# Kernel optimization log

Hardware: AMD Instinct MI355X
Metric: run time of the kernel (lower is better)

## Reference

```python
import jax, jax.numpy as jnp
import numpy as np

NUM_GROUPS = 32
EPS = 1e-6
NUM_HEADS = 8
HEAD_DIM = 64


def group_norm(x, gamma, beta):
    # x: [B, C, H, W]
    B, C, H, W = x.shape
    xg = x.reshape(B, NUM_GROUPS, C // NUM_GROUPS, H, W)
    mean = xg.mean(axis=(2, 3, 4), keepdims=True)
    var = xg.var(axis=(2, 3, 4), keepdims=True)
    xn = ((xg - mean) * jax.lax.rsqrt(var + EPS)).reshape(B, C, H, W)
    return xn * gamma[None, :, None, None] + beta[None, :, None, None]


def setup_inputs() -> dict:
    key = jax.random.key(0)
    ks = jax.random.split(key, 4)
    B, C, H, W = 8, 512, 32, 32
    hid = NUM_HEADS * HEAD_DIM  # 512
    x = jax.random.normal(ks[0], (B, C, H, W), dtype=jnp.float32)
    gamma = jnp.ones((C,), dtype=jnp.float32)
    beta = jnp.zeros((C,), dtype=jnp.float32)
    w_in = jax.random.normal(ks[1], (3 * hid, C), dtype=jnp.float32) * (1.0 / np.sqrt(C))
    b_in = jnp.zeros((3 * hid,), dtype=jnp.float32)
    w_out = jax.random.normal(ks[2], (C, hid), dtype=jnp.float32) * (1.0 / np.sqrt(hid))
    b_out = jnp.zeros((C,), dtype=jnp.float32)
    return {"x": x, "gamma": gamma, "beta": beta, "w_in": w_in, "b_in": b_in,
            "w_out": w_out, "b_out": b_out}


def reference(x, gamma, beta, w_in, b_in, w_out, b_out):
    B, C, H, W = x.shape
    n, c = NUM_HEADS, HEAD_DIM
    skip = x
    h = group_norm(x, gamma, beta)
    # 1x1 conv proj_in: [B, 3*n*c, H, W]
    qkv = jnp.einsum('oc,bchw->bohw', w_in, h) + b_in[None, :, None, None]
    qkv = qkv.reshape(B, 3, n, c, H * W)
    q, k, v = qkv[:, 0], qkv[:, 1], qkv[:, 2]  # each [B, n, c, HW]
    scale = 1.0 / np.sqrt(c)
    logits = jnp.einsum('bncq,bnck->bnqk', q, k) * scale  # [B, n, HW, HW]
    w = jax.nn.softmax(logits, axis=-1)
    out = jnp.einsum('bnqk,bnck->bncq', w, v)  # [B, n, c, HW]
    out = out.reshape(B, n * c, H, W)
    out = jnp.einsum('oc,bchw->bohw', w_out, out) + b_out[None, :, None, None]
    return out + skip
```

## Files before the change

kernel.cpp:

```cpp
#include <hip/hip_runtime.h>
#include <hip/hip_bf16.h>

#define B_    8
#define C_    512
#define HW_   1024
#define NG    32
#define GCH   16
#define EPSV  1e-6f

typedef __attribute__((ext_vector_type(8))) short short8;
typedef __attribute__((ext_vector_type(4))) short short4v;
typedef __attribute__((ext_vector_type(4))) float floatx4;

static __device__ __forceinline__ short f2bs(float f) {
  return __builtin_bit_cast(short, __float2bfloat16(f));
}
static __device__ __forceinline__ short4v pack4(float a, float b, float c, float d) {
  return (short4v){f2bs(a), f2bs(b), f2bs(c), f2bs(d)};
}
static __device__ __forceinline__ unsigned pk2(float a, float b) {
  return (unsigned)(unsigned short)f2bs(a) |
         ((unsigned)(unsigned short)f2bs(b) << 16);
}
#define MFMA(a, b, c) __builtin_amdgcn_mfma_f32_16x16x32_bf16((a), (b), (c), 0, 0, 0)

static __device__ __forceinline__ void glds16(const short* g, short* l) {
  __builtin_amdgcn_global_load_lds(
      (const __attribute__((address_space(1))) void*)g,
      (__attribute__((address_space(3))) void*)l, 16, 0, 0);
}

__global__ __launch_bounds__(256) void gn_cast_fused(
    const float* __restrict__ x, const float* __restrict__ gamma,
    const float* __restrict__ beta, short* __restrict__ ht,
    const float* __restrict__ w_in, short* __restrict__ wbf1,
    const float* __restrict__ w_out, short* __restrict__ wbf2) {
  int blk = blockIdx.x;
  int t = threadIdx.x;

  if (blk >= 256) {
    int i = (blk - 256) * 256 + t;
    const float* s; short* d; int j;
    if (i < 196608) { s = w_in; d = wbf1; j = i; }
    else            { s = w_out; d = wbf2; j = i - 196608; }
    float4 v = reinterpret_cast<const float4*>(s)[j];
    reinterpret_cast<short4v*>(d)[j] = pack4(v.x, v.y, v.z, v.w);
    return;
  }

  int b = blk >> 5, g = blk & 31;
  const float* xp = x + ((size_t)(b * C_) + g * GCH) * HW_;

  __shared__ float Ls[4 * 1040];
  __shared__ float rs_[4], rss_[4], st_[2];

  float s = 0.f, ss = 0.f;
  for (int i = 0; i < 16; i++) {
    float4 v = *reinterpret_cast<const float4*>(xp + (t + i * 256) * 4);
    s  += (v.x + v.y) + (v.z + v.w);
    ss += (v.x * v.x + v.y * v.y) + (v.z * v.z + v.w * v.w);
  }
  for (int o = 32; o > 0; o >>= 1) {
    s  += __shfl_down(s, o);
    ss += __shfl_down(ss, o);
  }
  int wid = t >> 6, lane = t & 63;
  if (lane == 0) { rs_[wid] = s; rss_[wid] = ss; }
  __syncthreads();
  if (t == 0) {
    float stot  = rs_[0] + rs_[1] + rs_[2] + rs_[3];
    float sstot = rss_[0] + rss_[1] + rss_[2] + rss_[3];
    float mean = stot / 16384.f;
    float var  = sstot / 16384.f - mean * mean;
    st_[0] = mean;
    st_[1] = rsqrtf(var + EPSV);
  }
  __syncthreads();

  int r = t >> 4, c4 = t & 15;
  int ch = g * GCH + r;
  float ga = gamma[ch] * st_[1];
  float be = beta[ch] - st_[0] * ga;
  int sq = t >> 2, cq = t & 3;

  for (int it = 0; it < 4; it++) {
    for (int sub = 0; sub < 4; sub++) {
      int s0 = (it * 4 + sub) * 64;
      float4 v = *reinterpret_cast<const float4*>(xp + r * HW_ + s0 + c4 * 4);
      float* L = Ls + sub * 1040;
      L[r * 65 + c4 * 4 + 0] = v.x * ga + be;
      L[r * 65 + c4 * 4 + 1] = v.y * ga + be;
      L[r * 65 + c4 * 4 + 2] = v.z * ga + be;
      L[r * 65 + c4 * 4 + 3] = v.w * ga + be;
    }
    __syncthreads();
    for (int sub = 0; sub < 4; sub++) {
      int s0 = (it * 4 + sub) * 64;
      const float* L = Ls + sub * 1040;
      float a0 = L[(cq * 4 + 0) * 65 + sq];
      float a1 = L[(cq * 4 + 1) * 65 + sq];
      float a2 = L[(cq * 4 + 2) * 65 + sq];
      float a3 = L[(cq * 4 + 3) * 65 + sq];
      *reinterpret_cast<short4v*>(
          ht + ((size_t)b * 1024 + s0 + sq) * 512 + g * GCH + cq * 4) =
          pack4(a0, a1, a2, a3);
    }
    __syncthreads();
  }
}

__global__ __launch_bounds__(256) void gemm_qkv(
    const short* __restrict__ Wb, const short* __restrict__ ht,
    const float* __restrict__ bias,
    short* __restrict__ Qt, short* __restrict__ Kt, short* __restrict__ Vn) {
  __shared__ short As[2][4096];
  __shared__ short Bs[2][4096];
  int bx = blockIdx.x, by = blockIdx.y, bb = blockIdx.z;
  int m0 = by * 128, n0 = bx * 128;
  int t = threadIdx.x;
  int w = t >> 6, lane = t & 63, n16 = lane & 15, quad = lane >> 4;
  int wm = (w >> 1) * 64, wn = (w & 1) * 64;

  const short* Wa = Wb + (size_t)(m0 + (t >> 2)) * 512 + (t & 3) * 8;
  const short* Xa = ht + (size_t)bb * 1024 * 512 +
                    (size_t)(n0 + (t >> 2)) * 512 + (t & 3) * 8;

#define STAGE(buf, kk)                                                \
  do {                                                                \
    glds16(Wa + (kk), &As[buf][t * 8]);                               \
    glds16(Wa + 64 * 512 + (kk), &As[buf][2048 + t * 8]);             \
    glds16(Xa + (kk), &Bs[buf][t * 8]);                               \
    glds16(Xa + 64 * 512 + (kk), &Bs[buf][2048 + t * 8]);             \
  } while (0)

  floatx4 acc[4][4];
  for (int i = 0; i < 4; i++)
    for (int j = 0; j < 4; j++) acc[i][j] = (floatx4){0.f, 0.f, 0.f, 0.f};

  STAGE(0, 0);
#pragma unroll 1
  for (int ks = 0; ks < 16; ks++) {
    int cur = ks & 1;
    __syncthreads();
    if (ks < 15) STAGE(cur ^ 1, (ks + 1) * 32);
    short8 a[4], b[4];
    for (int im = 0; im < 4; im++)
      a[im] = *reinterpret_cast<const short8*>(
          &As[cur][(wm + im * 16 + n16) * 32 + quad * 8]);
    for (int in = 0; in < 4; in++)
      b[in] = *reinterpret_cast<const short8*>(
          &Bs[cur][(wn + in * 16 + n16) * 32 + quad * 8]);
    for (int im = 0; im < 4; im++)
      for (int in = 0; in < 4; in++)
        acc[im][in] = MFMA(a[im], b[in], acc[im][in]);
  }
#undef STAGE

  if (m0 < 1024) {
    const bool isQ = (m0 < 512);
    short* base = isQ ? Qt : Kt;
    const float sc = isQ ? 0.125f : 1.0f;
    for (int im = 0; im < 4; im++) {
      int m = m0 + wm + im * 16 + quad * 4;
      int hh = (m >> 6) & 7, d0 = m & 63;
      float4 bi = *reinterpret_cast<const float4*>(&bias[m]);
      short* hb = base + (size_t)(bb * 8 + hh) * 1024 * 64 + d0;
      for (int in = 0; in < 4; in++) {
        int nn = n0 + wn + in * 16 + n16;
        *reinterpret_cast<short4v*>(hb + (size_t)nn * 64) =
            pack4((acc[im][in][0] + bi.x) * sc, (acc[im][in][1] + bi.y) * sc,
                  (acc[im][in][2] + bi.z) * sc, (acc[im][in][3] + bi.w) * sc);
      }
    }
  } else {
    for (int im = 0; im < 4; im++) {
      int m = m0 + wm + im * 16 + quad * 4;
      float4 bi = *reinterpret_cast<const float4*>(&bias[m]);
      int ch = m - 1024;
      for (int in = 0; in < 4; in++) {
        int nn = n0 + wn + in * 16 + n16;
        short* vp = Vn + (size_t)(bb * 512 + ch) * 1024 + nn;
        vp[0]    = f2bs(acc[im][in][0] + bi.x);
        vp[1024] = f2bs(acc[im][in][1] + bi.y);
        vp[2048] = f2bs(acc[im][in][2] + bi.z);
        vp[3072] = f2bs(acc[im][in][3] + bi.w);
      }
    }
  }
}

__global__ __launch_bounds__(256)
__attribute__((amdgpu_waves_per_eu(2))) void attn_mfma(
    const short* __restrict__ Qt, const short* __restrict__ Kt,
    const short* __restrict__ Vn, short* __restrict__ attnT) {
  int blk0 = blockIdx.x;
  int blk = (blk0 & 7) * 64 + (blk0 >> 3);
  int qb = blk & 7, h = (blk >> 3) & 7, b = blk >> 6;
  int t = threadIdx.x;
  int w = t >> 6, lane = t & 63, n16 = lane & 15, quad = lane >> 4;
  int q0 = qb * 128 + w * 32;
  int qhi = quad >> 1;
  int srcA = ((quad & 1) << 5) + n16;
  int srcB = srcA + 16;

  const short* Qp = Qt + (size_t)(b * 8 + h) * 1024 * 64;
  const short* Kp = Kt + (size_t)(b * 8 + h) * 1024 * 64;
  const short* Vp = Vn + (size_t)(b * 512 + h * 64) * 1024;

  short8 qa[2][2];
  for (int qt = 0; qt < 2; qt++)
    for (int f = 0; f < 2; f++)
      qa[qt][f] = *reinterpret_cast<const short8*>(
          Qp + (size_t)(q0 + qt * 16 + n16) * 64 + f * 32 + quad * 8);

  floatx4 O[2][4];
  float l[2] = {0.f, 0.f};
  for (int qt = 0; qt < 2; qt++)
    for (int i = 0; i < 4; i++) O[qt][i] = (floatx4){0.f, 0.f, 0.f, 0.f};

  short8 kf[8][2];
  short8 vv[4][2];

#pragma unroll 1
  for (int kt = 0; kt < 8; kt++) {
    int k0 = kt * 128;
#pragma unroll
    for (int nt = 0; nt < 8; nt++)
#pragma unroll
      for (int f = 0; f < 2; f++)
        kf[nt][f] = *reinterpret_cast<const short8*>(
            Kp + (size_t)(k0 + nt * 16 + n16) * 64 + f * 32 + quad * 8);

    short8 pa[2][4];
#pragma unroll
    for (int qt = 0; qt < 2; qt++) {
      floatx4 T[8];
#pragma unroll
      for (int nt = 0; nt < 8; nt++) {
        floatx4 s_ = (floatx4){0.f, 0.f, 0.f, 0.f};
        s_ = MFMA(kf[nt][0], qa[qt][0], s_);
        T[nt] = MFMA(kf[nt][1], qa[qt][1], s_);
      }
      unsigned u[8][2];
#pragma unroll
      for (int nt = 0; nt < 8; nt++) {
        float p0 = __expf(T[nt][0]);
        float p1 = __expf(T[nt][1]);
        float p2 = __expf(T[nt][2]);
        float p3 = __expf(T[nt][3]);
        l[qt] += (p0 + p1) + (p2 + p3);
        u[nt][0] = pk2(p0, p1);
        u[nt][1] = pk2(p2, p3);
      }
#pragma unroll
      for (int fr = 0; fr < 4; fr++) {
        unsigned a0 = (unsigned)__shfl((int)u[2 * fr + 0][0], srcA);
        unsigned a1 = (unsigned)__shfl((int)u[2 * fr + 1][0], srcA);
        unsigned b0 = (unsigned)__shfl((int)u[2 * fr + 0][1], srcA);
        unsigned b1 = (unsigned)__shfl((int)u[2 * fr + 1][1], srcA);
        unsigned c0 = (unsigned)__shfl((int)u[2 * fr + 0][0], srcB);
        unsigned c1 = (unsigned)__shfl((int)u[2 * fr + 1][0], srcB);
        unsigned d0 = (unsigned)__shfl((int)u[2 * fr + 0][1], srcB);
        unsigned d1 = (unsigned)__shfl((int)u[2 * fr + 1][1], srcB);
        uint4 wv;
        wv.x = qhi ? a1 : a0;
        wv.y = qhi ? b1 : b0;
        wv.z = qhi ? c1 : c0;
        wv.w = qhi ? d1 : d0;
        pa[qt][fr] = __builtin_bit_cast(short8, wv);
      }
    }

#pragma unroll
    for (int half = 0; half < 2; half++) {
#pragma unroll
      for (int nd = 0; nd < 4; nd++) {
        const short* vs = Vp + (size_t)(nd * 16 + n16) * 1024 + k0 +
                          half * 64 + quad * 8;
        vv[nd][0] = *reinterpret_cast<const short8*>(vs);
        vv[nd][1] = *reinterpret_cast<const short8*>(vs + 32);
      }
      __builtin_amdgcn_s_setprio(1);
#pragma unroll
      for (int qt = 0; qt < 2; qt++)
#pragma unroll
        for (int nd = 0; nd < 4; nd++) {
          O[qt][nd] = MFMA(pa[qt][2 * half + 0], vv[nd][0], O[qt][nd]);
          O[qt][nd] = MFMA(pa[qt][2 * half + 1], vv[nd][1], O[qt][nd]);
        }
      __builtin_amdgcn_s_setprio(0);
    }
  }

  for (int qt = 0; qt < 2; qt++) {
    float s = l[qt];
    s += __shfl_xor(s, 16);
    s += __shfl_xor(s, 32);
    for (int nd = 0; nd < 4; nd++)
      for (int r = 0; r < 4; r++) {
        float linv = 1.0f / __shfl(s, quad * 4 + r);
        int q = q0 + qt * 16 + quad * 4 + r;
        int ch = h * 64 + nd * 16 + n16;
        attnT[((size_t)b * 1024 + q) * 512 + ch] = f2bs(O[qt][nd][r] * linv);
      }
  }
}

__global__ __launch_bounds__(256) void gemm_out(
    const short* __restrict__ Wb, const short* __restrict__ Xt,
    const float* __restrict__ bias, const float* __restrict__ resid,
    float* __restrict__ out) {
  __shared__ short As[2][2048];
  __shared__ short Bs[2][2048];
  int bx = blockIdx.x, by = blockIdx.y, bb = blockIdx.z;
  int m0 = by * 64, n0 = bx * 64;
  int t = threadIdx.x;
  int w = t >> 6, lane = t & 63, n16 = lane & 15, quad = lane >> 4;
  int wm = (w >> 1) * 32, wn = (w & 1) * 32;

  const short* Wa = Wb + (size_t)(m0 + (t >> 2)) * 512 + (t & 3) * 8;
  const short* Xa = Xt + (size_t)bb * 1024 * 512 +
                    (size_t)(n0 + (t >> 2)) * 512 + (t & 3) * 8;

#define STAGE(buf, kk)                                                \
  do {                                                                \
    glds16(Wa + (kk), &As[buf][t * 8]);                               \
    glds16(Xa + (kk), &Bs[buf][t * 8]);                               \
  } while (0)

  floatx4 acc[2][2];
  for (int i = 0; i < 2; i++)
    for (int j = 0; j < 2; j++) acc[i][j] = (floatx4){0.f, 0.f, 0.f, 0.f};

  STAGE(0, 0);
#pragma unroll 1
  for (int ks = 0; ks < 16; ks++) {
    int cur = ks & 1;
    __syncthreads();
    if (ks < 15) STAGE(cur ^ 1, (ks + 1) * 32);
    short8 a[2], b[2];
    for (int im = 0; im < 2; im++)
      a[im] = *reinterpret_cast<const short8*>(
          &As[cur][(wm + im * 16 + n16) * 32 + quad * 8]);
    for (int in = 0; in < 2; in++)
      b[in] = *reinterpret_cast<const short8*>(
          &Bs[cur][(wn + in * 16 + n16) * 32 + quad * 8]);
    for (int im = 0; im < 2; im++)
      for (int in = 0; in < 2; in++)
        acc[im][in] = MFMA(a[im], b[in], acc[im][in]);
  }
#undef STAGE

  for (int im = 0; im < 2; im++) {
    int m = m0 + wm + im * 16 + quad * 4;
    float4 bi = *reinterpret_cast<const float4*>(&bias[m]);
    for (int in = 0; in < 2; in++) {
      int nn = n0 + wn + in * 16 + n16;
      size_t idx = ((size_t)bb * 512 + m) * 1024 + nn;
      out[idx]        = acc[im][in][0] + bi.x + resid[idx];
      out[idx + 1024] = acc[im][in][1] + bi.y + resid[idx + 1024];
      out[idx + 2048] = acc[im][in][2] + bi.z + resid[idx + 2048];
      out[idx + 3072] = acc[im][in][3] + bi.w + resid[idx + 3072];
    }
  }
}

extern "C" void kernel_launch(void* const* d_in, const int* in_sizes, int n_in,
                              void* d_out, int out_size, void* d_ws, size_t ws_size,
                              hipStream_t stream) {
  const float* x     = (const float*)d_in[0];
  const float* gamma = (const float*)d_in[1];
  const float* beta  = (const float*)d_in[2];
  const float* w_in  = (const float*)d_in[3];
  const float* b_in  = (const float*)d_in[4];
  const float* w_out = (const float*)d_in[5];
  const float* b_out = (const float*)d_in[6];
  float* out = (float*)d_out;

  char* ws = (char*)d_ws;
  short* ht    = (short*)ws;
  short* Qt    = (short*)(ws + (8u  << 20));
  short* Kt    = (short*)(ws + (16u << 20));
  short* Vn    = (short*)(ws + (24u << 20));
  short* attnT = (short*)(ws + (32u << 20));
  short* wbf1  = (short*)(ws + (40u << 20));
  short* wbf2  = (short*)(ws + (42u << 20));

  gn_cast_fused<<<1280, 256, 0, stream>>>(x, gamma, beta, ht,
                                          w_in, wbf1, w_out, wbf2);
  gemm_qkv<<<dim3(8, 12, B_), 256, 0, stream>>>(wbf1, ht, b_in, Qt, Kt, Vn);
  attn_mfma<<<512, 256, 0, stream>>>(Qt, Kt, Vn, attnT);
  gemm_out<<<dim3(16, 8, B_), 256, 0, stream>>>(wbf2, attnT, b_out, x, out);
}
```

Before: 184.6 us.

## Stage K/V tiles in swizzled LDS with double buffering in attention

```diff
diff --git a/kernel.cpp b/kernel.cpp
--- a/kernel.cpp
+++ b/kernel.cpp
@@ -189,16 +189,17 @@
   }
 }
 
-__global__ __launch_bounds__(256)
-__attribute__((amdgpu_waves_per_eu(2))) void attn_mfma(
+__global__ __launch_bounds__(256) void attn_mfma(
     const short* __restrict__ Qt, const short* __restrict__ Kt,
     const short* __restrict__ Vn, short* __restrict__ attnT) {
+  __shared__ short KT[2][4096];
+  __shared__ short VT[2][4096];
   int blk0 = blockIdx.x;
-  int blk = (blk0 & 7) * 64 + (blk0 >> 3);
-  int qb = blk & 7, h = (blk >> 3) & 7, b = blk >> 6;
+  int blk = (blk0 & 7) * 128 + (blk0 >> 3);
+  int qb = blk & 15, h = (blk >> 4) & 7, b = blk >> 7;
   int t = threadIdx.x;
   int w = t >> 6, lane = t & 63, n16 = lane & 15, quad = lane >> 4;
-  int q0 = qb * 128 + w * 32;
+  int q0 = qb * 64 + w * 16;
   int qhi = quad >> 1;
   int srcA = ((quad & 1) << 5) + n16;
   int srcB = srcA + 16;
@@ -207,101 +208,108 @@
   const short* Kp = Kt + (size_t)(b * 8 + h) * 1024 * 64;
   const short* Vp = Vn + (size_t)(b * 512 + h * 64) * 1024;
 
-  short8 qa[2][2];
-  for (int qt = 0; qt < 2; qt++)
-    for (int f = 0; f < 2; f++)
-      qa[qt][f] = *reinterpret_cast<const short8*>(
-          Qp + (size_t)(q0 + qt * 16 + n16) * 64 + f * 32 + quad * 8);
-
-  floatx4 O[2][4];
-  float l[2] = {0.f, 0.f};
-  for (int qt = 0; qt < 2; qt++)
-    for (int i = 0; i < 4; i++) O[qt][i] = (floatx4){0.f, 0.f, 0.f, 0.f};
-
-  short8 kf[8][2];
-  short8 vv[4][2];
-
+  short8 qa[2];
+  for (int f = 0; f < 2; f++)
+    qa[f] = *reinterpret_cast<const short8*>(
+        Qp + (size_t)(q0 + n16) * 64 + f * 32 + quad * 8);
+
+  floatx4 O[4];
+  float l = 0.f;
+  for (int i = 0; i < 4; i++) O[i] = (floatx4){0.f, 0.f, 0.f, 0.f};
+
+  int p0 = t * 16, p1 = 4096 + t * 16;
+  int r0 = p0 >> 7, c0 = (p0 & 127) ^ ((r0 & 7) << 4);
+  int r1 = p1 >> 7, c1 = (p1 & 127) ^ ((r1 & 7) << 4);
+
+#define STAGEKV(buf, ktv)                                                    \
+  do {                                                                       \
+    const char* Kb_ = (const char*)Kp + (ktv) * 8192;                        \
+    const char* Vb_ = (const char*)Vp + (ktv) * 128;                         \
+    glds16((const short*)(Kb_ + r0 * 128 + c0), &KT[buf][p0 >> 1]);          \
+    glds16((const short*)(Kb_ + r1 * 128 + c1), &KT[buf][p1 >> 1]);          \
+    glds16((const short*)(Vb_ + (size_t)r0 * 2048 + c0), &VT[buf][p0 >> 1]); \
+    glds16((const short*)(Vb_ + (size_t)r1 * 2048 + c1), &VT[buf][p1 >> 1]); \
+  } while (0)
+
+#define LDSOFF(row, colb) ((row) * 128 + (((colb) ^ (((row) & 7) << 4))))
+
+  STAGEKV(0, 0);
 #pragma unroll 1
-  for (int kt = 0; kt < 8; kt++) {
-    int k0 = kt * 128;
-#pragma unroll
-    for (int nt = 0; nt < 8; nt++)
-#pragma unroll
-      for (int f = 0; f < 2; f++)
+  for (int kt = 0; kt < 16; kt++) {
+    int cur = kt & 1;
+    __syncthreads();
+    if (kt < 15) STAGEKV(cur ^ 1, kt + 1);
+
+    short8 kf[4][2], v[4][2];
+#pragma unroll
+    for (int nt = 0; nt < 4; nt++)
+#pragma unroll
+      for (int f = 0; f < 2; f++) {
         kf[nt][f] = *reinterpret_cast<const short8*>(
-            Kp + (size_t)(k0 + nt * 16 + n16) * 64 + f * 32 + quad * 8);
-
-    short8 pa[2][4];
-#pragma unroll
-    for (int qt = 0; qt < 2; qt++) {
-      floatx4 T[8];
-#pragma unroll
-      for (int nt = 0; nt < 8; nt++) {
-        floatx4 s_ = (floatx4){0.f, 0.f, 0.f, 0.f};
-        s_ = MFMA(kf[nt][0], qa[qt][0], s_);
-        T[nt] = MFMA(kf[nt][1], qa[qt][1], s_);
+            (const char*)&KT[cur][0] +
+            LDSOFF(nt * 16 + n16, f * 64 + quad * 16));
+        v[nt][f] = *reinterpret_cast<const short8*>(
+            (const char*)&VT[cur][0] +
+            LDSOFF(nt * 16 + n16, f * 64 + quad * 16));
       }
-      unsigned u[8][2];
-#pragma unroll
-      for (int nt = 0; nt < 8; nt++) {
-        float p0 = __expf(T[nt][0]);
-        float p1 = __expf(T[nt][1]);
-        float p2 = __expf(T[nt][2]);
-        float p3 = __expf(T[nt][3]);
-        l[qt] += (p0 + p1) + (p2 + p3);
-        u[nt][0] = pk2(p0, p1);
-        u[nt][1] = pk2(p2, p3);
-      }
-#pragma unroll
-      for (int fr = 0; fr < 4; fr++) {
-        unsigned a0 = (unsigned)__shfl((int)u[2 * fr + 0][0], srcA);
-        unsigned a1 = (unsigned)__shfl((int)u[2 * fr + 1][0], srcA);
-        unsigned b0 = (unsigned)__shfl((int)u[2 * fr + 0][1], srcA);
-        unsigned b1 = (unsigned)__shfl((int)u[2 * fr + 1][1], srcA);
-        unsigned c0 = (unsigned)__shfl((int)u[2 * fr + 0][0], srcB);
-        unsigned c1 = (unsigned)__shfl((int)u[2 * fr + 1][0], srcB);
-        unsigned d0 = (unsigned)__shfl((int)u[2 * fr + 0][1], srcB);
-        unsigned d1 = (unsigned)__shfl((int)u[2 * fr + 1][1], srcB);
-        uint4 wv;
-        wv.x = qhi ? a1 : a0;
-        wv.y = qhi ? b1 : b0;
-        wv.z = qhi ? c1 : c0;
-        wv.w = qhi ? d1 : d0;
-        pa[qt][fr] = __builtin_bit_cast(short8, wv);
-      }
-    }
-
-#pragma unroll
-    for (int half = 0; half < 2; half++) {
-#pragma unroll
-      for (int nd = 0; nd < 4; nd++) {
-        const short* vs = Vp + (size_t)(nd * 16 + n16) * 1024 + k0 +
-                          half * 64 + quad * 8;
-        vv[nd][0] = *reinterpret_cast<const short8*>(vs);
-        vv[nd][1] = *reinterpret_cast<const short8*>(vs + 32);
-      }
-      __builtin_amdgcn_s_setprio(1);
-#pragma unroll
-      for (int qt = 0; qt < 2; qt++)
-#pragma unroll
-        for (int nd = 0; nd < 4; nd++) {
-          O[qt][nd] = MFMA(pa[qt][2 * half + 0], vv[nd][0], O[qt][nd]);
-          O[qt][nd] = MFMA(pa[qt][2 * half + 1], vv[nd][1], O[qt][nd]);
-        }
-      __builtin_amdgcn_s_setprio(0);
-    }
-  }
-
-  for (int qt = 0; qt < 2; qt++) {
-    float s = l[qt];
+
+    floatx4 T[4];
+#pragma unroll
+    for (int nt = 0; nt < 4; nt++) {
+      floatx4 s_ = (floatx4){0.f, 0.f, 0.f, 0.f};
+      s_ = MFMA(kf[nt][0], qa[0], s_);
+      T[nt] = MFMA(kf[nt][1], qa[1], s_);
+    }
+    unsigned u[4][2];
+#pragma unroll
+    for (int nt = 0; nt < 4; nt++) {
+      float p0_ = __expf(T[nt][0]);
+      float p1_ = __expf(T[nt][1]);
+      float p2_ = __expf(T[nt][2]);
+      float p3_ = __expf(T[nt][3]);
+      l += (p0_ + p1_) + (p2_ + p3_);
+      u[nt][0] = pk2(p0_, p1_);
+      u[nt][1] = pk2(p2_, p3_);
+    }
+    short8 pa[2];
+#pragma unroll
+    for (int f = 0; f < 2; f++) {
+      unsigned a0 = (unsigned)__shfl((int)u[2 * f + 0][0], srcA);
+      unsigned a1 = (unsigned)__shfl((int)u[2 * f + 1][0], srcA);
+      unsigned b0 = (unsigned)__shfl((int)u[2 * f + 0][1], srcA);
+      unsigned b1 = (unsigned)__shfl((int)u[2 * f + 1][1], srcA);
+      unsigned c0_ = (unsigned)__shfl((int)u[2 * f + 0][0], srcB);
+      unsigned c1_ = (unsigned)__shfl((int)u[2 * f + 1][0], srcB);
+      unsigned d0 = (unsigned)__shfl((int)u[2 * f + 0][1], srcB);
+      unsigned d1 = (unsigned)__shfl((int)u[2 * f + 1][1], srcB);
+      uint4 wv;
+      wv.x = qhi ? a1 : a0;
+      wv.y = qhi ? b1 : b0;
+      wv.z = qhi ? c1_ : c0_;
+      wv.w = qhi ? d1 : d0;
+      pa[f] = __builtin_bit_cast(short8, wv);
+    }
+    __builtin_amdgcn_s_setprio(1);
+#pragma unroll
+    for (int nd = 0; nd < 4; nd++) {
+      O[nd] = MFMA(pa[0], v[nd][0], O[nd]);
+      O[nd] = MFMA(pa[1], v[nd][1], O[nd]);
+    }
+    __builtin_amdgcn_s_setprio(0);
+  }
+#undef STAGEKV
+#undef LDSOFF
+
+  {
+    float s = l;
     s += __shfl_xor(s, 16);
     s += __shfl_xor(s, 32);
     for (int nd = 0; nd < 4; nd++)
       for (int r = 0; r < 4; r++) {
         float linv = 1.0f / __shfl(s, quad * 4 + r);
-        int q = q0 + qt * 16 + quad * 4 + r;
+        int q = q0 + quad * 4 + r;
         int ch = h * 64 + nd * 16 + n16;
-        attnT[((size_t)b * 1024 + q) * 512 + ch] = f2bs(O[qt][nd][r] * linv);
+        attnT[((size_t)b * 1024 + q) * 512 + ch] = f2bs(O[nd][r] * linv);
       }
   }
 }
@@ -389,6 +397,6 @@
   gn_cast_fused<<<1280, 256, 0, stream>>>(x, gamma, beta, ht,
                                           w_in, wbf1, w_out, wbf2);
   gemm_qkv<<<dim3(8, 12, B_), 256, 0, stream>>>(wbf1, ht, b_in, Qt, Kt, Vn);
-  attn_mfma<<<512, 256, 0, stream>>>(Qt, Kt, Vn, attnT);
+  attn_mfma<<<1024, 256, 0, stream>>>(Qt, Kt, Vn, attnT);
   gemm_out<<<dim3(16, 8, B_), 256, 0, stream>>>(wbf2, attnT, b_out, x, out);
 }
```

Result: faster. 159.5 us (-13.6%).
